# Optimization experiments

Hardware: AMD Instinct MI355X
Metric: run time of the kernel (lower is better)

Reference implementation:

```python
import jax, jax.numpy as jnp
import numpy as np


def setup_inputs() -> dict:
    key = jax.random.key(0)
    k1, k2, k3 = jax.random.split(key, 3)
    B, N, M, C = 4, 4096, 8192, 64
    PPU = 64.0  # points_per_unit
    xz = jax.random.normal(k1, (B, M, 1), dtype=jnp.float32) * 10.0  # grid locations
    z = jax.random.normal(k2, (B, C, M), dtype=jnp.float32)          # channels-first features
    x = jax.random.normal(k3, (B, N, 1), dtype=jnp.float32) * 10.0   # query locations
    log_scale = jnp.asarray(np.log(2.0 / PPU), dtype=jnp.float32)
    return {"xz": xz, "z": z, "x": x, "log_scale": log_scale}


def reference(xz, z, x, log_scale):
    # pairwise squared distances between x [B,N,1] and xz [B,M,1] -> [B,N,M]
    diff = x - jnp.swapaxes(xz, -1, -2)            # [B,N,M]
    dists2 = diff * diff
    # RBF weights (no normalization)
    weights = jnp.exp(-0.5 * dists2 / jnp.exp(2.0 * log_scale))  # [B,N,M]
    # z: [B,C,M] -> transpose -> [B,M,C]; weights @ z^T -> [B,N,C]
    out = jnp.einsum('bnm,bcm->bnc', weights, z)
    return out
```

## Files before the change

### kernel.cpp

```cpp
#include <hip/hip_runtime.h>
#include <math.h>

#define B 4
#define N 4096
#define M 8192
#define C 64
#define NB 2048
#define XMIN (-64.0f)
#define INV_BW 16.0f
#define CUT 10.0f
#define QG 16
#define NSUBP 4
#define NSUBQ 2

typedef __attribute__((ext_vector_type(8))) short short8;
typedef __attribute__((ext_vector_type(4))) float f32x4;

__device__ __forceinline__ int bucket_of(float v) {
    int k = (int)floorf((v - XMIN) * INV_BW);
    return min(max(k, 0), NB - 1);
}

__device__ __forceinline__ unsigned short f2bf(float f) {
    unsigned int u = __float_as_uint(f);
    return (unsigned short)((u + 0x7FFF + ((u >> 16) & 1)) >> 16);
}

__global__ __launch_bounds__(1024) void prep_kernel(
    const float* __restrict__ xz, const float* __restrict__ x,
    const float* __restrict__ z,
    int* __restrict__ part,
    unsigned short* __restrict__ zt)
{
    const int t   = threadIdx.x;
    const int blk = blockIdx.x;

    __shared__ int   h[NB];
    __shared__ float tile[64][65];

    if (blk < 24) {
        h[t] = 0; h[t + 1024] = 0;
        __syncthreads();
        const bool isQ = blk >= 16;
        const int  b   = isQ ? (blk - 16) >> 1 : blk >> 2;
        const int  sub = isQ ? (blk - 16) & 1  : blk & 3;
        const float* src = (isQ ? x + b * N : xz + b * M) + sub * 2048;
        float2 v2 = *(const float2*)(src + t * 2);
        atomicAdd(&h[bucket_of(v2.x)], 1);
        atomicAdd(&h[bucket_of(v2.y)], 1);
        __syncthreads();
        part[blk * NB + t]        = h[t];
        part[blk * NB + 1024 + t] = h[1024 + t];
    } else {
        const int tix = blk - 24;
        const int b   = tix >> 7;
        const int m0  = (tix & 127) * 64;
        const int m   = t & 63;
        #pragma unroll
        for (int k = 0; k < 4; ++k) {
            int c = (t >> 6) + 16 * k;
            tile[c][m] = z[((size_t)b * C + c) * M + m0 + m];
        }
        __syncthreads();
        const int j  = t >> 4;
        const int c4 = t & 15;
        ushort4 v4;
        v4.x = f2bf(tile[c4 * 4 + 0][j]);
        v4.y = f2bf(tile[c4 * 4 + 1][j]);
        v4.z = f2bf(tile[c4 * 4 + 2][j]);
        v4.w = f2bf(tile[c4 * 4 + 3][j]);
        ((ushort4*)zt)[((size_t)b * M + m0 + j) * 16 + c4] = v4;
    }
}

__global__ __launch_bounds__(256) void scat_kernel(
    const float* __restrict__ xz, const float* __restrict__ x,
    const int* __restrict__ part,
    int* __restrict__ bucket_start,
    float* __restrict__ xs,
    int* __restrict__ iord,
    float* __restrict__ qcs,
    int* __restrict__ qis)
{
    const int t    = threadIdx.x;
    const int lane = t & 63;
    const int w    = t >> 6;
    const int bid  = blockIdx.x;
    const bool isQ = bid >= 16;
    const int  b   = isQ ? (bid - 16) >> 1 : bid >> 2;
    const int  sub = isQ ? (bid - 16) & 1  : bid & 3;
    const int  nsub = isQ ? NSUBQ : NSUBP;
    const int  pb0  = isQ ? 16 + b * 2 : b * 4;
    const float* src = (isQ ? x + b * N : xz + b * M) + sub * 2048;

    __shared__ int base[NB];
    __shared__ int cnt[NB];
    __shared__ int wsum[4];

    int tot[8], mine[8];
    #pragma unroll
    for (int j = 0; j < 8; ++j) { tot[j] = 0; mine[j] = 0; }
    for (int s_ = 0; s_ < nsub; ++s_) {
        #pragma unroll
        for (int j = 0; j < 8; ++j) {
            const int v = part[(pb0 + s_) * NB + t * 8 + j];
            tot[j] += v;
            if (s_ < sub) mine[j] += v;
        }
    }
    int pre[8]; int tsum = 0;
    #pragma unroll
    for (int j = 0; j < 8; ++j) { pre[j] = tsum; tsum += tot[j]; }
    int s = tsum;
    #pragma unroll
    for (int off = 1; off < 64; off <<= 1) {
        int up = __shfl_up(s, off, 64);
        if (lane >= off) s += up;
    }
    if (lane == 63) wsum[w] = s;
    #pragma unroll
    for (int i = 0; i < 8; ++i) cnt[t + 256 * i] = 0;
    __syncthreads();
    int woff = 0;
    for (int i = 0; i < w; ++i) woff += wsum[i];
    const int excl = woff + s - tsum;
    #pragma unroll
    for (int j = 0; j < 8; ++j) base[t * 8 + j] = excl + pre[j] + mine[j];
    if (!isQ && sub == 0) {
        #pragma unroll
        for (int j = 0; j < 8; ++j)
            bucket_start[b * (NB + 1) + t * 8 + j] = excl + pre[j];
        if (t == 255) bucket_start[b * (NB + 1) + NB] = woff + s;
    }
    __syncthreads();

    #pragma unroll
    for (int j = 0; j < 2; ++j) {
        float4 v4 = *(const float4*)(src + t * 4 + j * 1024);
        float vv[4] = {v4.x, v4.y, v4.z, v4.w};
        #pragma unroll
        for (int c = 0; c < 4; ++c) {
            const int k    = bucket_of(vv[c]);
            const int slot = base[k] + atomicAdd(&cnt[k], 1);
            const int orig = sub * 2048 + t * 4 + j * 1024 + c;
            if (!isQ) {
                xs[b * M + slot]   = vv[c];
                iord[b * M + slot] = orig;
            } else {
                qcs[b * N + slot] = vv[c];
                qis[b * N + slot] = orig;
            }
        }
    }
}

__global__ __launch_bounds__(256) void gather_kernel(
    const float* __restrict__ log_scale,
    const int* __restrict__ bucket_start,
    const float* __restrict__ xs,
    const float* __restrict__ qcs,
    const int* __restrict__ qis,
    const int* __restrict__ iord,
    const unsigned short* __restrict__ zt,
    float* __restrict__ out)
{
    const int t    = threadIdx.x;
    const int lane = t & 63;
    const int w    = t >> 6;
    const int quad = lane >> 4;
    const int low4 = lane & 15;
    const int g  = blockIdx.x;
    const int b  = g >> 8;
    const int g0 = (g & 255) * QG;

    __shared__ unsigned short zr[64 * 64];
    __shared__ unsigned short wl[QG][72];
    __shared__ float qcS[QG];
    __shared__ int   qiS[QG];

    const float ls   = log_scale[0];
    const float coef = -0.5f * __expf(-2.0f * ls);
    const float R    = sqrtf(CUT / (-coef));

    if (t < QG) {
        qcS[t] = qcs[b * N + g0 + t];
        qiS[t] = qis[b * N + g0 + t];
    }

    const float qlo = qcs[b * N + g0];
    const float qhi = qcs[b * N + g0 + QG - 1];
    const int k0 = max(bucket_of(qlo - R) - 1, 0);
    const int k1 = min(bucket_of(qhi + R) + 1, NB - 1);
    const int s0 = bucket_start[b * (NB + 1) + k0];
    const int s1 = bucket_start[b * (NB + 1) + k1 + 1];
    const int e0 = s0 & ~63;
    const int e1 = (s1 + 63) & ~63;

    const int qw = w * 4 + quad;
    const int pg = low4;

    const float* xsb = xs + b * M;
    const int* iordb = iord + b * M;
    const unsigned short* ztb = zt + (size_t)b * M * C;

    const int ridx0 = (w * 2 + 0) * 8 + (lane >> 3);
    const int ridx1 = (w * 2 + 1) * 8 + (lane >> 3);
    int gmA = 0, gmB = 0;
    float4 xpA = {0.f, 0.f, 0.f, 0.f};
    if (e0 < e1) {
        gmA = iordb[e0 + ridx0];
        gmB = iordb[e0 + ridx1];
        xpA = *(const float4*)(xsb + e0 + pg * 4);
    }

    __syncthreads();
    const float qv = qcS[qw];

    f32x4 acc = {0.f, 0.f, 0.f, 0.f};

    for (int cs = e0; cs < e1; cs += 64) {
        __syncthreads();
        {
            const unsigned short* gpA = ztb + (size_t)gmA * C + (lane & 7) * 8;
            const unsigned short* gpB = ztb + (size_t)gmB * C + (lane & 7) * 8;
            __builtin_amdgcn_global_load_lds(
                (const __attribute__((address_space(1))) void*)gpA,
                (__attribute__((address_space(3))) void*)(zr + (w * 2 + 0) * 512),
                16, 0, 0);
            __builtin_amdgcn_global_load_lds(
                (const __attribute__((address_space(1))) void*)gpB,
                (__attribute__((address_space(3))) void*)(zr + (w * 2 + 1) * 512),
                16, 0, 0);
        }
        {
            float d0 = qv - xpA.x, d1 = qv - xpA.y;
            float d2 = qv - xpA.z, d3 = qv - xpA.w;
            ushort4 wv;
            wv.x = f2bf(__expf(coef * d0 * d0));
            wv.y = f2bf(__expf(coef * d1 * d1));
            wv.z = f2bf(__expf(coef * d2 * d2));
            wv.w = f2bf(__expf(coef * d3 * d3));
            *(ushort4*)&wl[qw][pg * 4] = wv;
        }
        if (cs + 64 < e1) {
            gmA = iordb[cs + 64 + ridx0];
            gmB = iordb[cs + 64 + ridx1];
            xpA = *(const float4*)(xsb + cs + 64 + pg * 4);
        }
        __syncthreads();
        #pragma unroll
        for (int kh = 0; kh < 2; ++kh) {
            short8 afrag = *(const short8*)&wl[low4][kh * 32 + quad * 8];
            short8 bfrag;
            #pragma unroll
            for (int j = 0; j < 8; ++j) {
                const int p = kh * 32 + quad * 8 + j;
                bfrag[j] = (short)zr[p * 64 + w * 16 + low4];
            }
            acc = __builtin_amdgcn_mfma_f32_16x16x32_bf16(afrag, bfrag, acc, 0, 0, 0);
        }
    }

    #pragma unroll
    for (int r = 0; r < 4; ++r) {
        const int q = quad * 4 + r;
        out[((size_t)b * N + qiS[q]) * C + w * 16 + low4] = acc[r];
    }
}

extern "C" void kernel_launch(void* const* d_in, const int* in_sizes, int n_in,
                              void* d_out, int out_size, void* d_ws, size_t ws_size,
                              hipStream_t stream) {
    const float* xz = (const float*)d_in[0];
    const float* z  = (const float*)d_in[1];
    const float* x  = (const float*)d_in[2];
    const float* ls = (const float*)d_in[3];
    float* out = (float*)d_out;

    char* ws = (char*)d_ws;
    size_t off = 0;
    auto alloc = [&](size_t bytes) { void* p = ws + off; off += (bytes + 255) & ~size_t(255); return p; };

    unsigned short* zt = (unsigned short*)alloc((size_t)B * M * C * sizeof(unsigned short));
    float* xs   = (float*)alloc(((size_t)B * M + 64) * sizeof(float));
    int*   iord = (int*)alloc((size_t)B * M * sizeof(int));
    float* qcs  = (float*)alloc((size_t)B * N * sizeof(float));
    int*   qis  = (int*)alloc((size_t)B * N * sizeof(int));
    int*   bst  = (int*)alloc((size_t)B * (NB + 1) * sizeof(int));
    int*   part = (int*)alloc((size_t)24 * NB * sizeof(int));

    prep_kernel<<<536, 1024, 0, stream>>>(xz, x, z, part, zt);
    scat_kernel<<<24, 256, 0, stream>>>(xz, x, part, bst, xs, iord, qcs, qis);
    gather_kernel<<<B * (N / QG), 256, 0, stream>>>(ls, bst, xs, qcs, qis, iord, zt, out);
}
```

Baseline: 81.96 us.

## Split histogram into tiny kernel and fuse scatter with z transpose

The histogram now runs in its own small 24-block kernel. The bucket scan and scatter are merged into the 536-block kernel that also transposes z to bf16, so the small serial scatter work overlaps the large transpose instead of running as a separate 24-block launch afterwards. The scatter blocks now use 1024 threads with 2 buckets per thread rather than 256 threads with 8. The cost is one more short launch at the start, and the transpose blocks now carry the larger shared-memory footprint of base and cnt, which may lower occupancy.

```diff
diff --git a/kernel.cpp b/kernel.cpp
--- a/kernel.cpp
+++ b/kernel.cpp
@@ -26,31 +26,99 @@
     return (unsigned short)((u + 0x7FFF + ((u >> 16) & 1)) >> 16);
 }
 
-__global__ __launch_bounds__(1024) void prep_kernel(
+__global__ __launch_bounds__(1024) void hist_kernel(
     const float* __restrict__ xz, const float* __restrict__ x,
-    const float* __restrict__ z,
-    int* __restrict__ part,
-    unsigned short* __restrict__ zt)
+    int* __restrict__ part)
 {
     const int t   = threadIdx.x;
     const int blk = blockIdx.x;
-
-    __shared__ int   h[NB];
+    __shared__ int h[NB];
+    h[t] = 0; h[t + 1024] = 0;
+    __syncthreads();
+    const bool isQ = blk >= 16;
+    const int  b   = isQ ? (blk - 16) >> 1 : blk >> 2;
+    const int  sub = isQ ? (blk - 16) & 1  : blk & 3;
+    const float* src = (isQ ? x + b * N : xz + b * M) + sub * 2048;
+    float2 v2 = *(const float2*)(src + t * 2);
+    atomicAdd(&h[bucket_of(v2.x)], 1);
+    atomicAdd(&h[bucket_of(v2.y)], 1);
+    __syncthreads();
+    part[blk * NB + t]        = h[t];
+    part[blk * NB + 1024 + t] = h[1024 + t];
+}
+
+__global__ __launch_bounds__(1024) void work_kernel(
+    const float* __restrict__ xz, const float* __restrict__ x,
+    const float* __restrict__ z,  const int* __restrict__ part,
+    int* __restrict__ bucket_start,
+    float* __restrict__ xs,
+    int* __restrict__ iord,
+    float* __restrict__ qcs,
+    int* __restrict__ qis,
+    unsigned short* __restrict__ zt)
+{
+    const int t    = threadIdx.x;
+    const int blk  = blockIdx.x;
+    const int lane = t & 63;
+    const int w    = t >> 6;
+
+    __shared__ int   base[NB];
+    __shared__ int   cnt[NB];
+    __shared__ int   wsum[16];
     __shared__ float tile[64][65];
 
     if (blk < 24) {
-        h[t] = 0; h[t + 1024] = 0;
-        __syncthreads();
         const bool isQ = blk >= 16;
         const int  b   = isQ ? (blk - 16) >> 1 : blk >> 2;
         const int  sub = isQ ? (blk - 16) & 1  : blk & 3;
+        const int  nsub = isQ ? NSUBQ : NSUBP;
+        const int  pb0  = isQ ? 16 + b * 2 : b * 4;
         const float* src = (isQ ? x + b * N : xz + b * M) + sub * 2048;
+
+        int tot0 = 0, tot1 = 0, mine0 = 0, mine1 = 0;
+        for (int s_ = 0; s_ < nsub; ++s_) {
+            const int v0 = part[(pb0 + s_) * NB + 2 * t];
+            const int v1 = part[(pb0 + s_) * NB + 2 * t + 1];
+            tot0 += v0; tot1 += v1;
+            if (s_ < sub) { mine0 += v0; mine1 += v1; }
+        }
+        const int tsum = tot0 + tot1;
+        int s = tsum;
+        #pragma unroll
+        for (int off = 1; off < 64; off <<= 1) {
+            int up = __shfl_up(s, off, 64);
+            if (lane >= off) s += up;
+        }
+        if (lane == 63) wsum[w] = s;
+        cnt[t] = 0; cnt[t + 1024] = 0;
+        __syncthreads();
+        int woff = 0;
+        for (int i = 0; i < w; ++i) woff += wsum[i];
+        const int excl = woff + s - tsum;
+        base[2 * t]     = excl + mine0;
+        base[2 * t + 1] = excl + tot0 + mine1;
+        if (!isQ && sub == 0) {
+            bucket_start[b * (NB + 1) + 2 * t]     = excl;
+            bucket_start[b * (NB + 1) + 2 * t + 1] = excl + tot0;
+            if (t == 1023) bucket_start[b * (NB + 1) + NB] = woff + s;
+        }
+        __syncthreads();
+
         float2 v2 = *(const float2*)(src + t * 2);
-        atomicAdd(&h[bucket_of(v2.x)], 1);
-        atomicAdd(&h[bucket_of(v2.y)], 1);
-        __syncthreads();
-        part[blk * NB + t]        = h[t];
-        part[blk * NB + 1024 + t] = h[1024 + t];
+        float vv[2] = {v2.x, v2.y};
+        #pragma unroll
+        for (int c = 0; c < 2; ++c) {
+            const int k    = bucket_of(vv[c]);
+            const int slot = base[k] + atomicAdd(&cnt[k], 1);
+            const int orig = sub * 2048 + t * 2 + c;
+            if (!isQ) {
+                xs[b * M + slot]   = vv[c];
+                iord[b * M + slot] = orig;
+            } else {
+                qcs[b * N + slot] = vv[c];
+                qis[b * N + slot] = orig;
+            }
+        }
     } else {
         const int tix = blk - 24;
         const int b   = tix >> 7;
@@ -70,87 +138,6 @@
         v4.z = f2bf(tile[c4 * 4 + 2][j]);
         v4.w = f2bf(tile[c4 * 4 + 3][j]);
         ((ushort4*)zt)[((size_t)b * M + m0 + j) * 16 + c4] = v4;
-    }
-}
-
-__global__ __launch_bounds__(256) void scat_kernel(
-    const float* __restrict__ xz, const float* __restrict__ x,
-    const int* __restrict__ part,
-    int* __restrict__ bucket_start,
-    float* __restrict__ xs,
-    int* __restrict__ iord,
-    float* __restrict__ qcs,
-    int* __restrict__ qis)
-{
-    const int t    = threadIdx.x;
-    const int lane = t & 63;
-    const int w    = t >> 6;
-    const int bid  = blockIdx.x;
-    const bool isQ = bid >= 16;
-    const int  b   = isQ ? (bid - 16) >> 1 : bid >> 2;
-    const int  sub = isQ ? (bid - 16) & 1  : bid & 3;
-    const int  nsub = isQ ? NSUBQ : NSUBP;
-    const int  pb0  = isQ ? 16 + b * 2 : b * 4;
-    const float* src = (isQ ? x + b * N : xz + b * M) + sub * 2048;
-
-    __shared__ int base[NB];
-    __shared__ int cnt[NB];
-    __shared__ int wsum[4];
-
-    int tot[8], mine[8];
-    #pragma unroll
-    for (int j = 0; j < 8; ++j) { tot[j] = 0; mine[j] = 0; }
-    for (int s_ = 0; s_ < nsub; ++s_) {
-        #pragma unroll
-        for (int j = 0; j < 8; ++j) {
-            const int v = part[(pb0 + s_) * NB + t * 8 + j];
-            tot[j] += v;
-            if (s_ < sub) mine[j] += v;
-        }
-    }
-    int pre[8]; int tsum = 0;
-    #pragma unroll
-    for (int j = 0; j < 8; ++j) { pre[j] = tsum; tsum += tot[j]; }
-    int s = tsum;
-    #pragma unroll
-    for (int off = 1; off < 64; off <<= 1) {
-        int up = __shfl_up(s, off, 64);
-        if (lane >= off) s += up;
-    }
-    if (lane == 63) wsum[w] = s;
-    #pragma unroll
-    for (int i = 0; i < 8; ++i) cnt[t + 256 * i] = 0;
-    __syncthreads();
-    int woff = 0;
-    for (int i = 0; i < w; ++i) woff += wsum[i];
-    const int excl = woff + s - tsum;
-    #pragma unroll
-    for (int j = 0; j < 8; ++j) base[t * 8 + j] = excl + pre[j] + mine[j];
-    if (!isQ && sub == 0) {
-        #pragma unroll
-        for (int j = 0; j < 8; ++j)
-            bucket_start[b * (NB + 1) + t * 8 + j] = excl + pre[j];
-        if (t == 255) bucket_start[b * (NB + 1) + NB] = woff + s;
-    }
-    __syncthreads();
-
-    #pragma unroll
-    for (int j = 0; j < 2; ++j) {
-        float4 v4 = *(const float4*)(src + t * 4 + j * 1024);
-        float vv[4] = {v4.x, v4.y, v4.z, v4.w};
-        #pragma unroll
-        for (int c = 0; c < 4; ++c) {
-            const int k    = bucket_of(vv[c]);
-            const int slot = base[k] + atomicAdd(&cnt[k], 1);
-            const int orig = sub * 2048 + t * 4 + j * 1024 + c;
-            if (!isQ) {
-                xs[b * M + slot]   = vv[c];
-                iord[b * M + slot] = orig;
-            } else {
-                qcs[b * N + slot] = vv[c];
-                qis[b * N + slot] = orig;
-            }
-        }
     }
 }
 
@@ -289,7 +276,7 @@
     int*   bst  = (int*)alloc((size_t)B * (NB + 1) * sizeof(int));
     int*   part = (int*)alloc((size_t)24 * NB * sizeof(int));
 
-    prep_kernel<<<536, 1024, 0, stream>>>(xz, x, z, part, zt);
-    scat_kernel<<<24, 256, 0, stream>>>(xz, x, part, bst, xs, iord, qcs, qis);
+    hist_kernel<<<24, 1024, 0, stream>>>(xz, x, part);
+    work_kernel<<<536, 1024, 0, stream>>>(xz, x, z, part, bst, xs, iord, qcs, qis, zt);
     gather_kernel<<<B * (N / QG), 256, 0, stream>>>(ls, bst, xs, qcs, qis, iord, zt, out);
 }
```

After: 81.75 us. Within noise of the previous version (-0.3%).
